# Performance work log

Hardware: AMD Instinct MI355X
Metric: run time of the kernel (lower is better)

Reference implementation:

```python
import jax, jax.numpy as jnp
import numpy as np

N_NODES = 100000
N_EDGES = 3200000
NUM_GRAPHS = 512


def _glorot(key, shape):
    fan_in, fan_out = shape[0], shape[1]
    lim = float(np.sqrt(6.0 / (fan_in + fan_out)))
    return jax.random.uniform(key, shape, jnp.float32, -lim, lim)


def setup_inputs() -> dict:
    key = jax.random.key(0)
    ks = jax.random.split(key, 12)
    x = jax.random.normal(ks[0], (N_NODES, 3), jnp.float32)
    edge_index = jax.random.randint(ks[1], (2, N_EDGES), 0, N_NODES, jnp.int64)
    batch = jnp.sort(jax.random.randint(ks[2], (N_NODES,), 0, NUM_GRAPHS, jnp.int64))
    return {
        'x': x,
        'edge_index': edge_index,
        'batch': batch,
        'W1': _glorot(ks[3], (3, 32)), 'b1': jnp.zeros((32,), jnp.float32),
        'W2': _glorot(ks[4], (32, 64)), 'b2': jnp.zeros((64,), jnp.float32),
        'W3': _glorot(ks[5], (64, 64)), 'b3': jnp.zeros((64,), jnp.float32),
        'lW1': _glorot(ks[6], (64, 32)), 'lb1': jnp.zeros((32,), jnp.float32),
        'lW2': _glorot(ks[7], (32, 5)), 'lb2': jnp.zeros((5,), jnp.float32),
    }


def gcn_conv(x, src, dst, W, b, n):
    # PyG GCNConv: add self-loops, symmetric deg^{-1/2} normalization,
    # linear transform then gather-scale-scatter aggregation.
    loop = jnp.arange(n, dtype=src.dtype)
    s = jnp.concatenate([src, loop])
    d = jnp.concatenate([dst, loop])
    deg = jax.ops.segment_sum(jnp.ones_like(d, dtype=x.dtype), d, num_segments=n)
    dinv = jnp.where(deg > 0, jax.lax.rsqrt(deg), 0.0)
    norm = dinv[s] * dinv[d]  # [E+N]
    h = x @ W                 # [N, out]
    out = jax.ops.segment_sum(h[s] * norm[:, None], d, num_segments=n)
    return out + b


def reference(x, edge_index, batch, W1, b1, W2, b2, W3, b3, lW1, lb1, lW2, lb2):
    src, dst = edge_index[0], edge_index[1]
    n = x.shape[0]
    h = jax.nn.relu(gcn_conv(x, src, dst, W1, b1, n))
    h = jax.nn.relu(gcn_conv(h, src, dst, W2, b2, n))
    h = gcn_conv(h, src, dst, W3, b3, n)
    pooled = jax.ops.segment_sum(h, batch, num_segments=NUM_GRAPHS)  # [G, 64]
    z = jax.nn.relu(pooled @ lW1 + lb1)
    z = z @ lW2 + lb2
    # original applies log_softmax over dim=0 (the graph axis)
    return jax.nn.log_softmax(z, axis=0)
```

## Files before the change

kernel.cpp:

```cpp
#include <hip/hip_runtime.h>
#include <hip/hip_fp16.h>

#define N_GRAPHS 512
#define NB 1563
#define KNODE 64
#define CAP 3072
#define EPW 8192
#define NWMAX 400
#define HCAP 2048


__global__ void k_part2(const int4* __restrict__ src4, const int4* __restrict__ dst4,
                        unsigned* __restrict__ ebuf2, unsigned* __restrict__ P, int E, int nw) {
    __shared__ int dstc[EPW];
    __shared__ unsigned hist[NB];
    __shared__ unsigned tsum[256];
    int w = blockIdx.x, t = threadIdx.x;
    int e0 = w * EPW;
    int cnt = E - e0 < EPW ? E - e0 : EPW;
    int cnt4 = cnt >> 2;
    for (int i = t; i < NB; i += 256) hist[i] = 0;
    __syncthreads();
    const int4* d4 = dst4 + (e0 >> 2);
    const int4* s4 = src4 + (e0 >> 2);
    for (int i = t; i < cnt4; i += 256) {
        int4 d = d4[i];
        dstc[4 * i + 0] = d.x; dstc[4 * i + 1] = d.y;
        dstc[4 * i + 2] = d.z; dstc[4 * i + 3] = d.w;
        atomicAdd(&hist[d.x >> 6], 1u);
        atomicAdd(&hist[d.y >> 6], 1u);
        atomicAdd(&hist[d.z >> 6], 1u);
        atomicAdd(&hist[d.w >> 6], 1u);
    }
    __syncthreads();
    const int PT7 = 7;
    unsigned loc[PT7];
    int base = t * PT7;
    unsigned s = 0;
#pragma unroll
    for (int k = 0; k < PT7; ++k) {
        int idx = base + k;
        unsigned v = (idx < NB) ? hist[idx] : 0u;
        loc[k] = s;
        s += v;
    }
    tsum[t] = s;
    __syncthreads();
    for (int off = 1; off < 256; off <<= 1) {
        unsigned u = (t >= off) ? tsum[t - off] : 0u;
        __syncthreads();
        tsum[t] += u;
        __syncthreads();
    }
    unsigned toff = tsum[t] - s;
#pragma unroll
    for (int k = 0; k < PT7; ++k) {
        int idx = base + k;
        if (idx < NB) {
            unsigned cb = ((k < PT7 - 1) ? loc[k + 1] : s) - loc[k];
            unsigned st = toff + loc[k];
            P[(size_t)w * NB + idx] = (st << 16) | cb;
        }
    }
    __syncthreads();
#pragma unroll
    for (int k = 0; k < PT7; ++k) {
        int idx = base + k;
        if (idx < NB) hist[idx] = toff + loc[k];
    }
    __syncthreads();
    for (int i = t; i < cnt4; i += 256) {
        int4 sv = s4[i];
#pragma unroll
        for (int q = 0; q < 4; ++q) {
            int d = dstc[4 * i + q];
            int svv = q == 0 ? sv.x : q == 1 ? sv.y : q == 2 ? sv.z : sv.w;
            int bkt = d >> 6;
            unsigned pos = atomicAdd(&hist[bkt], 1u);
            ebuf2[(size_t)e0 + pos] = (unsigned)svv | ((unsigned)(d & 63) << 20);
        }
    }
}


__global__ void kT(const unsigned* __restrict__ P, unsigned* __restrict__ PT, int nw) {
    __shared__ unsigned tile[32][33];
    int bw = blockIdx.x;
    int bb = blockIdx.y;
    int tx = threadIdx.x & 31, ty = threadIdx.x >> 5;
#pragma unroll
    for (int r = 0; r < 32; r += 8) {
        int w = bw * 32 + ty + r;
        int b = bb * 32 + tx;
        tile[ty + r][tx] = (w < nw && b < NB) ? P[(size_t)w * NB + b] : 0u;
    }
    __syncthreads();
#pragma unroll
    for (int r = 0; r < 32; r += 8) {
        int b = bb * 32 + ty + r;
        int w = bw * 32 + tx;
        if (b < NB && w < nw) PT[(size_t)b * nw + w] = tile[tx][ty + r];
    }
}


__global__ void k_csr2(const unsigned* __restrict__ ebuf2, const unsigned* __restrict__ PT,
                       unsigned* __restrict__ ebufF, int* __restrict__ gCnt,
                       int2* __restrict__ rows, float* __restrict__ dinv, int n, int nw) {
    __shared__ unsigned ec[CAP];
    __shared__ unsigned info[NWMAX];
    __shared__ unsigned coff[NWMAX];
    __shared__ unsigned tsum[256];
    __shared__ int bins[KNODE], pfx[KNODE];
    int b = blockIdx.x, t = threadIdx.x;
    for (int w = t; w < nw; w += 256) info[w] = PT[(size_t)b * nw + w];
    __syncthreads();
    unsigned l0, l1, s = 0;
    {
        int i0 = t * 2, i1 = t * 2 + 1;
        unsigned v0 = (i0 < nw) ? (info[i0] & 0xFFFFu) : 0u;
        unsigned v1 = (i1 < nw) ? (info[i1] & 0xFFFFu) : 0u;
        l0 = 0; l1 = v0; s = v0 + v1;
    }
    tsum[t] = s;
    __syncthreads();
    for (int off = 1; off < 256; off <<= 1) {
        unsigned u = (t >= off) ? tsum[t - off] : 0u;
        __syncthreads();
        tsum[t] += u;
        __syncthreads();
    }
    unsigned toff = tsum[t] - s;
    {
        int i0 = t * 2, i1 = t * 2 + 1;
        if (i0 < nw) coff[i0] = toff + l0;
        if (i1 < nw) coff[i1] = toff + l1;
    }
    __syncthreads();
    int total = (int)tsum[255];
    int cnt = total < CAP ? total : CAP;
    if (t == 0) gCnt[b] = cnt;
    for (int w = t; w < nw; w += 256) {
        unsigned inf = info[w];
        unsigned st = inf >> 16, c = inf & 0xFFFFu;
        unsigned d0 = coff[w];
        const unsigned* src = ebuf2 + (size_t)w * EPW + st;
        for (unsigned k = 0; k < c; ++k) {
            unsigned p = d0 + k;
            if (p < (unsigned)CAP) ec[p] = src[k];
        }
    }
    if (t < KNODE) bins[t] = 0;
    __syncthreads();
    for (int i = t; i < cnt; i += 256) atomicAdd(&bins[ec[i] >> 20], 1);
    __syncthreads();
    if (t == 0) {
        int a = 0;
        for (int i = 0; i < KNODE; ++i) { pfx[i] = a; a += bins[i]; }
    }
    __syncthreads();
    if (t < KNODE) {
        int node = b * KNODE + t;
        if (node < n) {
            rows[node] = make_int2(b * CAP + pfx[t], bins[t]);
            dinv[node] = rsqrtf((float)(bins[t] + 1));
        }
    }
    if (t < KNODE) bins[t] = pfx[t];
    __syncthreads();
    for (int i = t; i < cnt; i += 256) {
        unsigned p = ec[i];
        int pp = atomicAdd(&bins[p >> 20], 1);
        ebufF[(size_t)b * CAP + pp] = p & 0xFFFFFu;
    }
}


__global__ void k_pre1(const float* __restrict__ x, const float* __restrict__ dinv,
                       float4* __restrict__ ts0, int n) {
    int i = blockIdx.x * 256 + threadIdx.x;
    if (i >= n) return;
    float d = dinv[i];
    ts0[i] = make_float4(d * x[3 * i], d * x[3 * i + 1], d * x[3 * i + 2], 0.f);
}


__global__ void k_agg1(const float4* __restrict__ ts0, const unsigned* __restrict__ esrc,
                       const int2* __restrict__ rows, const float* __restrict__ dinv,
                       float4* __restrict__ o1, int n) {
    int node = blockIdx.x * 256 + threadIdx.x;
    if (node >= n) return;
    int2 rc = rows[node];
    int s0 = rc.x, deg = rc.y;
    float4 a = ts0[node];
    int e = 0;
    for (; e + 4 <= deg; e += 4) {
        unsigned i0 = esrc[s0 + e + 0];
        unsigned i1 = esrc[s0 + e + 1];
        unsigned i2 = esrc[s0 + e + 2];
        unsigned i3 = esrc[s0 + e + 3];
        float4 v0 = ts0[i0], v1 = ts0[i1], v2 = ts0[i2], v3 = ts0[i3];
        a.x += v0.x + v1.x + v2.x + v3.x;
        a.y += v0.y + v1.y + v2.y + v3.y;
        a.z += v0.z + v1.z + v2.z + v3.z;
    }
    for (; e < deg; ++e) {
        float4 v = ts0[esrc[s0 + e]];
        a.x += v.x; a.y += v.y; a.z += v.z;
    }
    float d = dinv[node];
    o1[node] = make_float4(d * a.x, d * a.y, d * a.z, 0.f);
}


__global__ void k_t1(const float4* __restrict__ o1, const float* __restrict__ W1,
                     const float* __restrict__ b1, const float* __restrict__ dinv,
                     uint4* __restrict__ ts1, int n) {
    __shared__ float sW[96];
    __shared__ float sb[32];
    int t = threadIdx.x;
    if (t < 96) sW[t] = W1[t];
    if (t < 32) sb[t] = b1[t];
    __syncthreads();
    int ln = t >> 2, c = t & 3;
    int node = blockIdx.x * 64 + ln;
    if (node >= n) return;
    float4 o = o1[node];
    float d = dinv[node];
    float r[8];
#pragma unroll
    for (int k = 0; k < 8; ++k) {
        int j = c * 8 + k;
        float h = o.x * sW[j] + o.y * sW[32 + j] + o.z * sW[64 + j] + sb[j];
        r[k] = fmaxf(h, 0.f) * d;
    }
    __half2 h0 = __floats2half2_rn(r[0], r[1]);
    __half2 h1 = __floats2half2_rn(r[2], r[3]);
    __half2 h2 = __floats2half2_rn(r[4], r[5]);
    __half2 h3 = __floats2half2_rn(r[6], r[7]);
    uint4 w;
    w.x = *(unsigned*)&h0; w.y = *(unsigned*)&h1;
    w.z = *(unsigned*)&h2; w.w = *(unsigned*)&h3;
    ts1[(size_t)node * 4 + c] = w;
}


template <int LPN>
__global__ void k_aggN(const uint4* __restrict__ ts, const unsigned* __restrict__ ebuf,
                       const int* __restrict__ gCnt, const int2* __restrict__ rows,
                       const float* __restrict__ dinv, uint4* __restrict__ out, int n) {
    __shared__ unsigned eidx[HCAP];
    __shared__ int cursor;
    int blk = blockIdx.x;
    int b = blk >> 1, half = blk & 1;
    int n0 = b * KNODE + half * 32;
    if (n0 >= n) return;
    int t = threadIdx.x;
    int bBase = b * CAP;
    int cntb = gCnt[b];
    if (cntb > CAP) cntb = CAP;
    int startL = rows[n0].x - bBase;
    int endL;
    int nmid = b * KNODE + 32;
    if (half == 0 && nmid < n) endL = rows[nmid].x - bBase;
    else endL = cntb;
    int myCnt = endL - startL;
    if (myCnt > HCAP) myCnt = HCAP;
    const unsigned* esrc = ebuf + bBase + startL;
    for (int k = t; k < myCnt; k += 128) eidx[k] = esrc[k];
    if (t == 0) cursor = 0;
    __syncthreads();

    int lane = t & (LPN - 1);
    for (;;) {
        int my;
        if (lane == 0) my = atomicAdd(&cursor, 1);
        my = __shfl(my, (t / LPN) * LPN, 64);
        if (my >= 32) break;
        int node = n0 + my;
        if (node >= n) continue;
        int2 rc = rows[node];
        int ls = rc.x - bBase - startL;
        int deg = rc.y;
        if (ls + deg > myCnt) deg = myCnt - ls > 0 ? myCnt - ls : 0;
        float2 a0, a1, a2, a3;
        {
            uint4 sv = ts[(size_t)node * LPN + lane];
            a0 = __half22float2(*(__half2*)&sv.x);
            a1 = __half22float2(*(__half2*)&sv.y);
            a2 = __half22float2(*(__half2*)&sv.z);
            a3 = __half22float2(*(__half2*)&sv.w);
        }
        int e = 0;
        for (; e + 4 <= deg; e += 4) {
            uint4 v0 = ts[(size_t)eidx[ls + e + 0] * LPN + lane];
            uint4 v1 = ts[(size_t)eidx[ls + e + 1] * LPN + lane];
            uint4 v2 = ts[(size_t)eidx[ls + e + 2] * LPN + lane];
            uint4 v3 = ts[(size_t)eidx[ls + e + 3] * LPN + lane];
            float2 f;
            f = __half22float2(*(__half2*)&v0.x); a0.x += f.x; a0.y += f.y;
            f = __half22float2(*(__half2*)&v0.y); a1.x += f.x; a1.y += f.y;
            f = __half22float2(*(__half2*)&v0.z); a2.x += f.x; a2.y += f.y;
            f = __half22float2(*(__half2*)&v0.w); a3.x += f.x; a3.y += f.y;
            f = __half22float2(*(__half2*)&v1.x); a0.x += f.x; a0.y += f.y;
            f = __half22float2(*(__half2*)&v1.y); a1.x += f.x; a1.y += f.y;
            f = __half22float2(*(__half2*)&v1.z); a2.x += f.x; a2.y += f.y;
            f = __half22float2(*(__half2*)&v1.w); a3.x += f.x; a3.y += f.y;
            f = __half22float2(*(__half2*)&v2.x); a0.x += f.x; a0.y += f.y;
            f = __half22float2(*(__half2*)&v2.y); a1.x += f.x; a1.y += f.y;
            f = __half22float2(*(__half2*)&v2.z); a2.x += f.x; a2.y += f.y;
            f = __half22float2(*(__half2*)&v2.w); a3.x += f.x; a3.y += f.y;
            f = __half22float2(*(__half2*)&v3.x); a0.x += f.x; a0.y += f.y;
            f = __half22float2(*(__half2*)&v3.y); a1.x += f.x; a1.y += f.y;
            f = __half22float2(*(__half2*)&v3.z); a2.x += f.x; a2.y += f.y;
            f = __half22float2(*(__half2*)&v3.w); a3.x += f.x; a3.y += f.y;
        }
        for (; e < deg; ++e) {
            uint4 v = ts[(size_t)eidx[ls + e] * LPN + lane];
            float2 f;
            f = __half22float2(*(__half2*)&v.x); a0.x += f.x; a0.y += f.y;
            f = __half22float2(*(__half2*)&v.y); a1.x += f.x; a1.y += f.y;
            f = __half22float2(*(__half2*)&v.z); a2.x += f.x; a2.y += f.y;
            f = __half22float2(*(__half2*)&v.w); a3.x += f.x; a3.y += f.y;
        }
        float dd = dinv[node];
        __half2 o0 = __floats2half2_rn(dd * a0.x, dd * a0.y);
        __half2 o1 = __floats2half2_rn(dd * a1.x, dd * a1.y);
        __half2 o2 = __floats2half2_rn(dd * a2.x, dd * a2.y);
        __half2 o3 = __floats2half2_rn(dd * a3.x, dd * a3.y);
        uint4 w;
        w.x = *(unsigned*)&o0; w.y = *(unsigned*)&o1;
        w.z = *(unsigned*)&o2; w.w = *(unsigned*)&o3;
        out[(size_t)node * LPN + lane] = w;
    }
}


__global__ void k_t2(const uint4* __restrict__ o2, const float* __restrict__ W2,
                     const float* __restrict__ b2, const float* __restrict__ dinv,
                     uint4* __restrict__ ts2, int n) {
    __shared__ uint4 sO[128];
    __shared__ float sW[32 * 64];
    __shared__ float sb[64];
    int t = threadIdx.x;
    for (int i = t; i < 32 * 64; i += 256) sW[i] = W2[i];
    if (t < 64) sb[t] = b2[t];
    int node0 = blockIdx.x * 32;
    if (t < 128) {
        int nd = node0 + (t >> 2);
        sO[t] = (nd < n) ? o2[(size_t)node0 * 4 + t] : make_uint4(0, 0, 0, 0);
    }
    __syncthreads();
    int ln = t >> 3, c = t & 7;
    int node = node0 + ln;
    if (node >= n) return;
    const __half2* sOh = (const __half2*)sO;
    float acc[8];
#pragma unroll
    for (int k = 0; k < 8; ++k) acc[k] = sb[c * 8 + k];
#pragma unroll
    for (int i2 = 0; i2 < 16; ++i2) {
        float2 av = __half22float2(sOh[ln * 16 + i2]);
        const float* w0 = &sW[(2 * i2) * 64 + c * 8];
        const float* w1 = &sW[(2 * i2 + 1) * 64 + c * 8];
#pragma unroll
        for (int k = 0; k < 8; ++k) acc[k] += av.x * w0[k] + av.y * w1[k];
    }
    float d = dinv[node];
    float r[8];
#pragma unroll
    for (int k = 0; k < 8; ++k) r[k] = fmaxf(acc[k], 0.f) * d;
    __half2 h0 = __floats2half2_rn(r[0], r[1]);
    __half2 h1 = __floats2half2_rn(r[2], r[3]);
    __half2 h2 = __floats2half2_rn(r[4], r[5]);
    __half2 h3 = __floats2half2_rn(r[6], r[7]);
    uint4 w;
    w.x = *(unsigned*)&h0; w.y = *(unsigned*)&h1;
    w.z = *(unsigned*)&h2; w.w = *(unsigned*)&h3;
    ts2[(size_t)node * 8 + c] = w;
}


__global__ void k_pool(const __half2* __restrict__ h, const int* __restrict__ batch,
                       float* __restrict__ pooled, float* __restrict__ cntf, int n) {
    const int NBK = 32;
    int lane = threadIdx.x & 31;
    int sub = threadIdx.x >> 5;
    int n0 = (blockIdx.x * 8 + sub) * NBK;
    if (n0 >= n) return;
    int nend = n0 + NBK < n ? n0 + NBK : n;
    float2 acc = make_float2(0.f, 0.f);
    float rc = 0.f;
    int gcur = batch[n0];
    for (int i = n0; i < nend; ++i) {
        int g = batch[i];
        if (g != gcur) {
            atomicAdd(&pooled[gcur * 64 + 2 * lane], acc.x);
            atomicAdd(&pooled[gcur * 64 + 2 * lane + 1], acc.y);
            if (lane == 0) atomicAdd(&cntf[gcur], rc);
            acc = make_float2(0.f, 0.f);
            rc = 0.f;
            gcur = g;
        }
        float2 v = __half22float2(h[(size_t)i * 32 + lane]);
        acc.x += v.x;
        acc.y += v.y;
        rc += 1.f;
    }
    atomicAdd(&pooled[gcur * 64 + 2 * lane], acc.x);
    atomicAdd(&pooled[gcur * 64 + 2 * lane + 1], acc.y);
    if (lane == 0) atomicAdd(&cntf[gcur], rc);
}


#define GPB 4
__global__ void k_z(const float* __restrict__ P, const float* __restrict__ cntf,
                    const float* __restrict__ W3, const float* __restrict__ b3,
                    const float* __restrict__ lW1, const float* __restrict__ lb1,
                    const float* __restrict__ lW2, const float* __restrict__ lb2,
                    float* __restrict__ z) {
    __shared__ float sW3[64 * 64];
    __shared__ float sW1[64 * 32];
    __shared__ float sW2[32 * 5];
    __shared__ float sb3[64], sb1[32], sb2[5];
    __shared__ float sP[GPB][64];
    __shared__ float sH[GPB][64];
    __shared__ float sT[GPB][32];
    int t = threadIdx.x;
    for (int i = t; i < 64 * 64; i += 256) sW3[i] = W3[i];
    for (int i = t; i < 64 * 32; i += 256) sW1[i] = lW1[i];
    for (int i = t; i < 32 * 5; i += 256) sW2[i] = lW2[i];
    if (t < 64) sb3[t] = b3[t];
    if (t < 32) sb1[t] = lb1[t];
    if (t < 5) sb2[t] = lb2[t];
    int g0 = blockIdx.x * GPB;
    for (int i = t; i < GPB * 64; i += 256) sP[i >> 6][i & 63] = P[(size_t)g0 * 64 + i];
    __syncthreads();
    int lg = t >> 6;
    int j = t & 63;
    int g = g0 + lg;
    float cg = cntf[g];
    float a = cg * sb3[j];
#pragma unroll 8
    for (int i = 0; i < 64; ++i) a += sP[lg][i] * sW3[i * 64 + j];
    sH[lg][j] = a;
    __syncthreads();
    if (j < 32) {
        float a2 = sb1[j];
#pragma unroll 8
        for (int i = 0; i < 64; ++i) a2 += sH[lg][i] * sW1[i * 32 + j];
        sT[lg][j] = fmaxf(a2, 0.f);
    }
    __syncthreads();
    if (j < 5) {
        float a3 = sb2[j];
#pragma unroll
        for (int i = 0; i < 32; ++i) a3 += sT[lg][i] * sW2[i * 5 + j];
        z[g * 5 + j] = a3;
    }
}


__global__ void k_lsm(const float* __restrict__ z, float* __restrict__ out) {
    __shared__ float red[512];
    int g = threadIdx.x;
#pragma unroll
    for (int c = 0; c < 5; ++c) {
        float v = z[g * 5 + c];
        red[g] = v;
        __syncthreads();
        for (int off = 256; off > 0; off >>= 1) {
            if (g < off) red[g] = fmaxf(red[g], red[g + off]);
            __syncthreads();
        }
        float m = red[0];
        __syncthreads();
        red[g] = expf(v - m);
        __syncthreads();
        for (int off = 256; off > 0; off >>= 1) {
            if (g < off) red[g] += red[g + off];
            __syncthreads();
        }
        float lse = m + logf(red[0]);
        __syncthreads();
        out[g * 5 + c] = v - lse;
    }
}


extern "C" void kernel_launch(void* const* d_in, const int* in_sizes, int n_in,
                              void* d_out, int out_size, void* d_ws, size_t ws_size,
                              hipStream_t stream) {
    const float* x   = (const float*)d_in[0];
    const int* ei    = (const int*)d_in[1];
    const int* batch = (const int*)d_in[2];
    const float* W1  = (const float*)d_in[3];
    const float* b1  = (const float*)d_in[4];
    const float* W2  = (const float*)d_in[5];
    const float* b2  = (const float*)d_in[6];
    const float* W3  = (const float*)d_in[7];
    const float* b3  = (const float*)d_in[8];
    const float* lW1 = (const float*)d_in[9];
    const float* lb1 = (const float*)d_in[10];
    const float* lW2 = (const float*)d_in[11];
    const float* lb2 = (const float*)d_in[12];

    const int N = in_sizes[0] / 3;
    const int E = in_sizes[1] / 2;
    const int* src = ei;
    const int* dst = ei + E;
    const int nw = (E + EPW - 1) / EPW;

    char* ws = (char*)d_ws;
    size_t off = 0;
    auto alloc = [&](size_t bytes) -> void* {
        void* p = ws + off;
        off = (off + bytes + 255) & ~(size_t)255;
        return p;
    };

    int*      gCnt    = (int*)alloc((size_t)NB * 4);
    float*    dinv    = (float*)alloc((size_t)N * 4);
    int2*     rows    = (int2*)alloc((size_t)N * 8);
    unsigned* ebuf2   = (unsigned*)alloc((size_t)nw * EPW * 4);
    unsigned* P       = (unsigned*)alloc((size_t)nw * NB * 4);
    unsigned* PT      = (unsigned*)alloc((size_t)NB * nw * 4);
    unsigned* ebufF   = (unsigned*)alloc((size_t)NB * CAP * 4);
    uint4*    ts1     = (uint4*)alloc((size_t)N * 4 * 16);
    uint4*    o2      = (uint4*)alloc((size_t)N * 4 * 16);
    uint4*    ts2     = (uint4*)alloc((size_t)N * 8 * 16);
    float*    pooledP = (float*)alloc((size_t)N_GRAPHS * 64 * 4);
    float*    cntf    = (float*)alloc((size_t)N_GRAPHS * 4);
    float*    zbuf    = (float*)alloc((size_t)N_GRAPHS * 5 * 4);
    float4*   ts0     = (float4*)P;
    float4*   o1      = (float4*)PT;
    uint4*    o3      = (uint4*)ebuf2;

    hipMemsetAsync(pooledP, 0, (size_t)N_GRAPHS * 64 * 4, stream);
    hipMemsetAsync(cntf, 0, (size_t)N_GRAPHS * 4, stream);

    k_part2<<<nw, 256, 0, stream>>>((const int4*)src, (const int4*)dst, ebuf2, P, E, nw);
    dim3 gT((nw + 31) / 32, (NB + 31) / 32);
    kT<<<gT, 256, 0, stream>>>(P, PT, nw);
    k_csr2<<<NB, 256, 0, stream>>>(ebuf2, PT, ebufF, gCnt, rows, dinv, N, nw);

    k_pre1<<<(N + 255) / 256, 256, 0, stream>>>(x, dinv, ts0, N);
    k_agg1<<<(N + 255) / 256, 256, 0, stream>>>(ts0, ebufF, rows, dinv, o1, N);
    k_t1<<<(N + 63) / 64, 256, 0, stream>>>(o1, W1, b1, dinv, ts1, N);

    k_aggN<4><<<NB * 2, 128, 0, stream>>>(ts1, ebufF, gCnt, rows, dinv, o2, N);
    k_t2<<<(N + 31) / 32, 256, 0, stream>>>(o2, W2, b2, dinv, ts2, N);

    k_aggN<8><<<NB * 2, 128, 0, stream>>>(ts2, ebufF, gCnt, rows, dinv, o3, N);

    k_pool<<<(N + 8 * 32 - 1) / (8 * 32), 256, 0, stream>>>((const __half2*)o3, batch,
                                                            pooledP, cntf, N);
    k_z<<<N_GRAPHS / GPB, 256, 0, stream>>>(pooledP, cntf, W3, b3, lW1, lb1, lW2, lb2, zbuf);
    k_lsm<<<1, 512, 0, stream>>>(zbuf, (float*)d_out);
}
```

Measured before the change: 240.5 us.

## Fuse layer-1 aggregation with W1 transform and layer-2 aggregation with W2 transform

Merges the layer-1 gather kernel with its dense 3x32 transform, and the layer-2 fp16 gather with the 32x64 transform. The layer-2 kernel reuses the shared edge-index buffer to stage per-node aggregates and W2 as fp16. This removes two kernel launches and the round trips of the o1 and o2 intermediates through global memory. In exchange, the layer-2 block does more serial work per thread (16 accumulators over 32 inputs), and W2 is reloaded and converted in every block, which may lower occupancy or add latency.

```diff
diff --git a/kernel.cpp b/kernel.cpp
--- a/kernel.cpp
+++ b/kernel.cpp
@@ -185,10 +185,17 @@
 }
 
 
-__global__ void k_agg1(const float4* __restrict__ ts0, const unsigned* __restrict__ esrc,
-                       const int2* __restrict__ rows, const float* __restrict__ dinv,
-                       float4* __restrict__ o1, int n) {
-    int node = blockIdx.x * 256 + threadIdx.x;
+__global__ void k_l1(const float4* __restrict__ ts0, const unsigned* __restrict__ esrc,
+                     const int2* __restrict__ rows, const float* __restrict__ dinv,
+                     const float* __restrict__ W1, const float* __restrict__ b1,
+                     uint4* __restrict__ ts1, int n) {
+    __shared__ float sW[96];
+    __shared__ float sb[32];
+    int t = threadIdx.x;
+    if (t < 96) sW[t] = W1[t];
+    if (t < 32) sb[t] = b1[t];
+    __syncthreads();
+    int node = blockIdx.x * 256 + t;
     if (node >= n) return;
     int2 rc = rows[node];
     int s0 = rc.x, deg = rc.y;
@@ -209,39 +216,152 @@
         a.x += v.x; a.y += v.y; a.z += v.z;
     }
     float d = dinv[node];
-    o1[node] = make_float4(d * a.x, d * a.y, d * a.z, 0.f);
-}
-
-
-__global__ void k_t1(const float4* __restrict__ o1, const float* __restrict__ W1,
-                     const float* __restrict__ b1, const float* __restrict__ dinv,
-                     uint4* __restrict__ ts1, int n) {
-    __shared__ float sW[96];
-    __shared__ float sb[32];
+    float ox = d * a.x, oy = d * a.y, oz = d * a.z;
+#pragma unroll
+    for (int c = 0; c < 4; ++c) {
+        float r[8];
+#pragma unroll
+        for (int k = 0; k < 8; ++k) {
+            int j = c * 8 + k;
+            float h = ox * sW[j] + oy * sW[32 + j] + oz * sW[64 + j] + sb[j];
+            r[k] = fmaxf(h, 0.f) * d;
+        }
+        __half2 h0 = __floats2half2_rn(r[0], r[1]);
+        __half2 h1 = __floats2half2_rn(r[2], r[3]);
+        __half2 h2 = __floats2half2_rn(r[4], r[5]);
+        __half2 h3 = __floats2half2_rn(r[6], r[7]);
+        uint4 w;
+        w.x = *(unsigned*)&h0; w.y = *(unsigned*)&h1;
+        w.z = *(unsigned*)&h2; w.w = *(unsigned*)&h3;
+        ts1[(size_t)node * 4 + c] = w;
+    }
+}
+
+
+__global__ void k_l2(const uint4* __restrict__ ts, const unsigned* __restrict__ ebuf,
+                     const int* __restrict__ gCnt, const int2* __restrict__ rows,
+                     const float* __restrict__ dinv, const float* __restrict__ W2,
+                     const float* __restrict__ b2, uint4* __restrict__ ts2, int n) {
+    __shared__ unsigned smem[HCAP];
+    __shared__ float sb2[64];
+    int blk = blockIdx.x;
+    int b = blk >> 1, half = blk & 1;
+    int n0 = b * KNODE + half * 32;
+    if (n0 >= n) return;
     int t = threadIdx.x;
-    if (t < 96) sW[t] = W1[t];
-    if (t < 32) sb[t] = b1[t];
-    __syncthreads();
-    int ln = t >> 2, c = t & 3;
-    int node = blockIdx.x * 64 + ln;
-    if (node >= n) return;
-    float4 o = o1[node];
-    float d = dinv[node];
-    float r[8];
+    if (t < 64) sb2[t] = b2[t];
+    int bBase = b * CAP;
+    int cntb = gCnt[b];
+    if (cntb > CAP) cntb = CAP;
+    int startL = rows[n0].x - bBase;
+    int endL;
+    int nmid = b * KNODE + 32;
+    if (half == 0 && nmid < n) endL = rows[nmid].x - bBase;
+    else endL = cntb;
+    int myCnt = endL - startL;
+    if (myCnt > HCAP) myCnt = HCAP;
+    const unsigned* esrc = ebuf + bBase + startL;
+    for (int k = t; k < myCnt; k += 128) smem[k] = esrc[k];
+    __syncthreads();
+
+    int lane = t & 3;
+    int g = t >> 2;
+    int node = n0 + g;
+    float2 a0 = make_float2(0.f, 0.f), a1 = a0, a2 = a0, a3 = a0;
+    int ls = 0, deg = 0;
+    bool valid = node < n;
+    if (valid) {
+        int2 rc = rows[node];
+        ls = rc.x - bBase - startL;
+        deg = rc.y;
+        if (ls + deg > myCnt) deg = myCnt - ls > 0 ? myCnt - ls : 0;
+        uint4 sv = ts[(size_t)node * 4 + lane];
+        a0 = __half22float2(*(__half2*)&sv.x);
+        a1 = __half22float2(*(__half2*)&sv.y);
+        a2 = __half22float2(*(__half2*)&sv.z);
+        a3 = __half22float2(*(__half2*)&sv.w);
+        int e = 0;
+        for (; e + 4 <= deg; e += 4) {
+            uint4 v0 = ts[(size_t)smem[ls + e + 0] * 4 + lane];
+            uint4 v1 = ts[(size_t)smem[ls + e + 1] * 4 + lane];
+            uint4 v2 = ts[(size_t)smem[ls + e + 2] * 4 + lane];
+            uint4 v3 = ts[(size_t)smem[ls + e + 3] * 4 + lane];
+            float2 f;
+            f = __half22float2(*(__half2*)&v0.x); a0.x += f.x; a0.y += f.y;
+            f = __half22float2(*(__half2*)&v0.y); a1.x += f.x; a1.y += f.y;
+            f = __half22float2(*(__half2*)&v0.z); a2.x += f.x; a2.y += f.y;
+            f = __half22float2(*(__half2*)&v0.w); a3.x += f.x; a3.y += f.y;
+            f = __half22float2(*(__half2*)&v1.x); a0.x += f.x; a0.y += f.y;
+            f = __half22float2(*(__half2*)&v1.y); a1.x += f.x; a1.y += f.y;
+            f = __half22float2(*(__half2*)&v1.z); a2.x += f.x; a2.y += f.y;
+            f = __half22float2(*(__half2*)&v1.w); a3.x += f.x; a3.y += f.y;
+            f = __half22float2(*(__half2*)&v2.x); a0.x += f.x; a0.y += f.y;
+            f = __half22float2(*(__half2*)&v2.y); a1.x += f.x; a1.y += f.y;
+            f = __half22float2(*(__half2*)&v2.z); a2.x += f.x; a2.y += f.y;
+            f = __half22float2(*(__half2*)&v2.w); a3.x += f.x; a3.y += f.y;
+            f = __half22float2(*(__half2*)&v3.x); a0.x += f.x; a0.y += f.y;
+            f = __half22float2(*(__half2*)&v3.y); a1.x += f.x; a1.y += f.y;
+            f = __half22float2(*(__half2*)&v3.z); a2.x += f.x; a2.y += f.y;
+            f = __half22float2(*(__half2*)&v3.w); a3.x += f.x; a3.y += f.y;
+        }
+        for (; e < deg; ++e) {
+            uint4 v = ts[(size_t)smem[ls + e] * 4 + lane];
+            float2 f;
+            f = __half22float2(*(__half2*)&v.x); a0.x += f.x; a0.y += f.y;
+            f = __half22float2(*(__half2*)&v.y); a1.x += f.x; a1.y += f.y;
+            f = __half22float2(*(__half2*)&v.z); a2.x += f.x; a2.y += f.y;
+            f = __half22float2(*(__half2*)&v.w); a3.x += f.x; a3.y += f.y;
+        }
+        float dd = dinv[node];
+        a0.x *= dd; a0.y *= dd; a1.x *= dd; a1.y *= dd;
+        a2.x *= dd; a2.y *= dd; a3.x *= dd; a3.y *= dd;
+    }
+    __syncthreads();
+
+    float* sO = (float*)smem;
+    __half* sW2h = (__half*)(smem + 1024);
+    if (valid) {
+        int fb = lane * 8;
+        sO[g * 32 + fb + 0] = a0.x; sO[g * 32 + fb + 1] = a0.y;
+        sO[g * 32 + fb + 2] = a1.x; sO[g * 32 + fb + 3] = a1.y;
+        sO[g * 32 + fb + 4] = a2.x; sO[g * 32 + fb + 5] = a2.y;
+        sO[g * 32 + fb + 6] = a3.x; sO[g * 32 + fb + 7] = a3.y;
+    } else {
+        int fb = lane * 8;
+#pragma unroll
+        for (int k = 0; k < 8; ++k) sO[g * 32 + fb + k] = 0.f;
+    }
+    for (int i = t; i < 32 * 64; i += 128) sW2h[i] = __float2half(W2[i]);
+    __syncthreads();
+
+    if (!valid) return;
+    int c16 = lane * 16;
+    float acc[16];
+#pragma unroll
+    for (int k = 0; k < 16; ++k) acc[k] = sb2[c16 + k];
+    const float* myO = &sO[g * 32];
+#pragma unroll 4
+    for (int i = 0; i < 32; ++i) {
+        float av = myO[i];
+        const __half* wr = &sW2h[i * 64 + c16];
+#pragma unroll
+        for (int k = 0; k < 16; ++k) acc[k] += av * __half2float(wr[k]);
+    }
+    float dd = dinv[node];
+    __half2 hh[8];
 #pragma unroll
     for (int k = 0; k < 8; ++k) {
-        int j = c * 8 + k;
-        float h = o.x * sW[j] + o.y * sW[32 + j] + o.z * sW[64 + j] + sb[j];
-        r[k] = fmaxf(h, 0.f) * d;
-    }
-    __half2 h0 = __floats2half2_rn(r[0], r[1]);
-    __half2 h1 = __floats2half2_rn(r[2], r[3]);
-    __half2 h2 = __floats2half2_rn(r[4], r[5]);
-    __half2 h3 = __floats2half2_rn(r[6], r[7]);
-    uint4 w;
-    w.x = *(unsigned*)&h0; w.y = *(unsigned*)&h1;
-    w.z = *(unsigned*)&h2; w.w = *(unsigned*)&h3;
-    ts1[(size_t)node * 4 + c] = w;
+        float rx = fmaxf(acc[2 * k], 0.f) * dd;
+        float ry = fmaxf(acc[2 * k + 1], 0.f) * dd;
+        hh[k] = __floats2half2_rn(rx, ry);
+    }
+    uint4 w0, w1;
+    w0.x = *(unsigned*)&hh[0]; w0.y = *(unsigned*)&hh[1];
+    w0.z = *(unsigned*)&hh[2]; w0.w = *(unsigned*)&hh[3];
+    w1.x = *(unsigned*)&hh[4]; w1.y = *(unsigned*)&hh[5];
+    w1.z = *(unsigned*)&hh[6]; w1.w = *(unsigned*)&hh[7];
+    ts2[(size_t)node * 8 + lane * 2 + 0] = w0;
+    ts2[(size_t)node * 8 + lane * 2 + 1] = w1;
 }
 
 
@@ -336,51 +456,6 @@
 }
 
 
-__global__ void k_t2(const uint4* __restrict__ o2, const float* __restrict__ W2,
-                     const float* __restrict__ b2, const float* __restrict__ dinv,
-                     uint4* __restrict__ ts2, int n) {
-    __shared__ uint4 sO[128];
-    __shared__ float sW[32 * 64];
-    __shared__ float sb[64];
-    int t = threadIdx.x;
-    for (int i = t; i < 32 * 64; i += 256) sW[i] = W2[i];
-    if (t < 64) sb[t] = b2[t];
-    int node0 = blockIdx.x * 32;
-    if (t < 128) {
-        int nd = node0 + (t >> 2);
-        sO[t] = (nd < n) ? o2[(size_t)node0 * 4 + t] : make_uint4(0, 0, 0, 0);
-    }
-    __syncthreads();
-    int ln = t >> 3, c = t & 7;
-    int node = node0 + ln;
-    if (node >= n) return;
-    const __half2* sOh = (const __half2*)sO;
-    float acc[8];
-#pragma unroll
-    for (int k = 0; k < 8; ++k) acc[k] = sb[c * 8 + k];
-#pragma unroll
-    for (int i2 = 0; i2 < 16; ++i2) {
-        float2 av = __half22float2(sOh[ln * 16 + i2]);
-        const float* w0 = &sW[(2 * i2) * 64 + c * 8];
-        const float* w1 = &sW[(2 * i2 + 1) * 64 + c * 8];
-#pragma unroll
-        for (int k = 0; k < 8; ++k) acc[k] += av.x * w0[k] + av.y * w1[k];
-    }
-    float d = dinv[node];
-    float r[8];
-#pragma unroll
-    for (int k = 0; k < 8; ++k) r[k] = fmaxf(acc[k], 0.f) * d;
-    __half2 h0 = __floats2half2_rn(r[0], r[1]);
-    __half2 h1 = __floats2half2_rn(r[2], r[3]);
-    __half2 h2 = __floats2half2_rn(r[4], r[5]);
-    __half2 h3 = __floats2half2_rn(r[6], r[7]);
-    uint4 w;
-    w.x = *(unsigned*)&h0; w.y = *(unsigned*)&h1;
-    w.z = *(unsigned*)&h2; w.w = *(unsigned*)&h3;
-    ts2[(size_t)node * 8 + c] = w;
-}
-
-
 __global__ void k_pool(const __half2* __restrict__ h, const int* __restrict__ batch,
                        float* __restrict__ pooled, float* __restrict__ cntf, int n) {
     const int NBK = 32;
@@ -527,13 +602,11 @@
     unsigned* PT      = (unsigned*)alloc((size_t)NB * nw * 4);
     unsigned* ebufF   = (unsigned*)alloc((size_t)NB * CAP * 4);
     uint4*    ts1     = (uint4*)alloc((size_t)N * 4 * 16);
-    uint4*    o2      = (uint4*)alloc((size_t)N * 4 * 16);
     uint4*    ts2     = (uint4*)alloc((size_t)N * 8 * 16);
     float*    pooledP = (float*)alloc((size_t)N_GRAPHS * 64 * 4);
     float*    cntf    = (float*)alloc((size_t)N_GRAPHS * 4);
     float*    zbuf    = (float*)alloc((size_t)N_GRAPHS * 5 * 4);
     float4*   ts0     = (float4*)P;
-    float4*   o1      = (float4*)PT;
     uint4*    o3      = (uint4*)ebuf2;
 
     hipMemsetAsync(pooledP, 0, (size_t)N_GRAPHS * 64 * 4, stream);
@@ -545,11 +618,9 @@
     k_csr2<<<NB, 256, 0, stream>>>(ebuf2, PT, ebufF, gCnt, rows, dinv, N, nw);
 
     k_pre1<<<(N + 255) / 256, 256, 0, stream>>>(x, dinv, ts0, N);
-    k_agg1<<<(N + 255) / 256, 256, 0, stream>>>(ts0, ebufF, rows, dinv, o1, N);
-    k_t1<<<(N + 63) / 64, 256, 0, stream>>>(o1, W1, b1, dinv, ts1, N);
-
-    k_aggN<4><<<NB * 2, 128, 0, stream>>>(ts1, ebufF, gCnt, rows, dinv, o2, N);
-    k_t2<<<(N + 31) / 32, 256, 0, stream>>>(o2, W2, b2, dinv, ts2, N);
+    k_l1<<<(N + 255) / 256, 256, 0, stream>>>(ts0, ebufF, rows, dinv, W1, b1, ts1, N);
+
+    k_l2<<<NB * 2, 128, 0, stream>>>(ts1, ebufF, gCnt, rows, dinv, W2, b2, ts2, N);
 
     k_aggN<8><<<NB * 2, 128, 0, stream>>>(ts2, ebufF, gCnt, rows, dinv, o3, N);
 
```

Result: faster. 233.9 us (-2.7%).
